# Kernel tuning notes

Measured on AMD Instinct MI355X. Metric: run time of the kernel, lower is better.

The kernel has to match this reference:

```python
import jax, jax.numpy as jnp
import numpy as np

N_NODES = 100000
N_EDGES = 1600000
IN_DIM = 128
HID_DIM = 64
OUT_DIM = 64


def setup_inputs() -> dict:
    key = jax.random.key(0)
    ks = jax.random.split(key, 8)
    x = jax.random.normal(ks[0], (N_NODES, IN_DIM), dtype=jnp.float32)
    edge_index = jax.random.randint(ks[1], (2, N_EDGES), 0, N_NODES, dtype=jnp.int64)
    edge_weight = jax.random.uniform(ks[2], (N_EDGES,), dtype=jnp.float32)  # cached PPMI values
    # Glorot-style params for the two PPMIConv layers
    W1 = jax.random.normal(ks[3], (IN_DIM, HID_DIM), dtype=jnp.float32) * (1.0 / np.sqrt(IN_DIM))
    b1 = jnp.zeros((HID_DIM,), dtype=jnp.float32)
    W2 = jax.random.normal(ks[4], (HID_DIM, OUT_DIM), dtype=jnp.float32) * (1.0 / np.sqrt(HID_DIM))
    b2 = jnp.zeros((OUT_DIM,), dtype=jnp.float32)
    return {"x": x, "edge_index": edge_index, "edge_weight": edge_weight,
            "W1": W1, "b1": b1, "W2": W2, "b2": b2}


def _gcn_norm(edge_index, edge_weight, num_nodes):
    # symmetric normalization of (PPMI) edge weights: D^{-1/2} A D^{-1/2}
    row, col = edge_index[0], edge_index[1]
    deg = jax.ops.segment_sum(edge_weight, row, num_segments=num_nodes)
    deg_inv_sqrt = jnp.where(deg > 0, jax.lax.rsqrt(jnp.maximum(deg, 1e-12)), 0.0)
    return deg_inv_sqrt[row] * edge_weight * deg_inv_sqrt[col]


def _ppmi_conv(x, W, b, edge_index, norm, num_nodes):
    h = x @ W                                   # [N, D_out] transform
    msg = h[edge_index[0]] * norm[:, None]      # [E, D_out] gather + weight
    out = jax.ops.segment_sum(msg, edge_index[1], num_segments=num_nodes)  # scatter-add
    return out + b


def reference(x, edge_index, edge_weight, W1, b1, W2, b2):
    n = x.shape[0]
    norm = _gcn_norm(edge_index, edge_weight, n)
    h = _ppmi_conv(x, W1, b1, edge_index, norm, n)
    h = jax.nn.relu(h)
    h = _ppmi_conv(h, W2, b2, edge_index, norm, n)
    return h
```

## Files before the change

kernel.cpp:

```cpp
#include <hip/hip_runtime.h>
#include <hip/hip_fp16.h>

#define N_NODES 100000
#define N_EDGES 1600000
#define IN_DIM 128
#define HID_DIM 64
#define OUT_DIM 64
#define NBKT 196
#define BSH 9
#define BMSK 511
#define NBLK 512
#define CHUNK 3125
#define MROW (NBKT * NBLK)

typedef _Float16 half8 __attribute__((ext_vector_type(8)));
typedef float f32x4 __attribute__((ext_vector_type(4)));

__global__ void count_kernel(const int* __restrict__ rows, const int* __restrict__ cols,
                             int* __restrict__ M) {
    __shared__ unsigned hc[NBKT], hr[NBKT];
    for (int i = threadIdx.x; i < NBKT; i += 256) { hc[i] = 0; hr[i] = 0; }
    __syncthreads();
    const int s = blockIdx.x * CHUNK;
    const int e = min(s + CHUNK, N_EDGES);
    for (int i = s + threadIdx.x; i < e; i += 256) {
        atomicAdd(&hr[rows[i] >> BSH], 1u);
        atomicAdd(&hc[cols[i] >> BSH], 1u);
    }
    __syncthreads();
    for (int i = threadIdx.x; i < NBKT; i += 256) {
        M[i * NBLK + blockIdx.x] = (int)hc[i];
        M[MROW + i * NBLK + blockIdx.x] = (int)hr[i];
    }
}

__global__ void block_sum_kernel(const int* __restrict__ counts, int* __restrict__ partials, int n) {
    __shared__ int sh[256];
    int base = blockIdx.x * 1024;
    int s = 0;
    for (int i = threadIdx.x; i < 1024; i += 256) {
        int idx = base + i;
        s += (idx < n) ? counts[idx] : 0;
    }
    sh[threadIdx.x] = s;
    __syncthreads();
    for (int off = 128; off > 0; off >>= 1) {
        if (threadIdx.x < off) sh[threadIdx.x] += sh[threadIdx.x + off];
        __syncthreads();
    }
    if (threadIdx.x == 0) partials[blockIdx.x] = sh[0];
}

__global__ void scan_partials_kernel(int* __restrict__ p, int nb) {
    __shared__ int sh[256];
    int t = threadIdx.x;
    int v = (t < nb) ? p[t] : 0;
    sh[t] = v;
    __syncthreads();
    for (int off = 1; off < 256; off <<= 1) {
        int add = (t >= off) ? sh[t - off] : 0;
        __syncthreads();
        sh[t] += add;
        __syncthreads();
    }
    if (t < nb) p[t] = sh[t] - v;
}

__global__ void scan_final_kernel(const int* __restrict__ counts, const int* __restrict__ partials,
                                  int* __restrict__ offsets, int n) {
    __shared__ int sh[256];
    int t = threadIdx.x;
    int idx0 = blockIdx.x * 1024 + t * 4;
    int v[4];
    int s = 0;
#pragma unroll
    for (int j = 0; j < 4; ++j) {
        int id = idx0 + j;
        v[j] = (id < n) ? counts[id] : 0;
        s += v[j];
    }
    sh[t] = s;
    __syncthreads();
    for (int off = 1; off < 256; off <<= 1) {
        int add = (t >= off) ? sh[t - off] : 0;
        __syncthreads();
        sh[t] += add;
        __syncthreads();
    }
    int run = sh[t] - s + partials[blockIdx.x];
#pragma unroll
    for (int j = 0; j < 4; ++j) {
        int id = idx0 + j;
        if (id < n) offsets[id] = run;
        run += v[j];
    }
    if (idx0 <= n - 1 && n - 1 < idx0 + 4) offsets[n] = run;
}

__global__ __launch_bounds__(256) void scatter_kernel(
        const int* __restrict__ rows, const int* __restrict__ cols,
        const float* __restrict__ w, const int* __restrict__ M, const int* __restrict__ Ms,
        unsigned long long* __restrict__ pkA, unsigned* __restrict__ pkR) {
    __shared__ unsigned long long pay[CHUNK];
    __shared__ unsigned char bkt[CHUNK + 3];
    __shared__ unsigned scn[256];
    __shared__ unsigned base[NBKT], cur[NBKT], gbase[NBKT];
    const int blk = blockIdx.x, t = threadIdx.x;
    const int s = blk * CHUNK;

    unsigned cnt = (t < NBKT) ? (unsigned)M[t * NBLK + blk] : 0;
    scn[t] = cnt;
    __syncthreads();
    for (int off = 1; off < 256; off <<= 1) {
        unsigned a = (t >= off) ? scn[t - off] : 0;
        __syncthreads();
        scn[t] += a;
        __syncthreads();
    }
    if (t < NBKT) {
        unsigned b0 = scn[t] - cnt;
        base[t] = b0; cur[t] = b0;
        gbase[t] = (unsigned)Ms[t * NBLK + blk];
    }
    __syncthreads();
    for (int i = s + t; i < s + CHUNK; i += 256) {
        int r = rows[i], c = cols[i];
        unsigned b = (unsigned)c >> BSH;
        unsigned p = atomicAdd(&cur[b], 1u);
        pay[p] = ((unsigned long long)__float_as_uint(w[i]) << 32) |
                 (unsigned)(((c & BMSK) << 17) | r);
        bkt[p] = (unsigned char)b;
    }
    __syncthreads();
    for (int i = t; i < CHUNK; i += 256) {
        unsigned b = bkt[i];
        pkA[gbase[b] + (i - base[b])] = pay[i];
    }
    __syncthreads();

    cnt = (t < NBKT) ? (unsigned)M[MROW + t * NBLK + blk] : 0;
    scn[t] = cnt;
    __syncthreads();
    for (int off = 1; off < 256; off <<= 1) {
        unsigned a = (t >= off) ? scn[t - off] : 0;
        __syncthreads();
        scn[t] += a;
        __syncthreads();
    }
    if (t < NBKT) {
        unsigned b0 = scn[t] - cnt;
        base[t] = b0; cur[t] = b0;
        gbase[t] = (unsigned)Ms[MROW + t * NBLK + blk] - (unsigned)N_EDGES;
    }
    __syncthreads();
    unsigned* pay32 = (unsigned*)pay;
    for (int i = s + t; i < s + CHUNK; i += 256) {
        int r = rows[i];
        unsigned b = (unsigned)r >> BSH;
        unsigned p = atomicAdd(&cur[b], 1u);
        unsigned short hw = __half_as_ushort(__float2half(w[i]));
        pay32[p] = ((unsigned)hw << 16) | (unsigned)(r & BMSK);
        bkt[p] = (unsigned char)b;
    }
    __syncthreads();
    for (int i = t; i < CHUNK; i += 256) {
        unsigned b = bkt[i];
        pkR[gbase[b] + (i - base[b])] = pay32[i];
    }
}

__global__ void deg_reduce_kernel(const unsigned* __restrict__ pkR,
                                  const int* __restrict__ Ms, float* __restrict__ dis) {
    __shared__ float acc[512];
    const int b = blockIdx.x;
    const int t = threadIdx.x;
    acc[t] = 0.f; acc[t + 256] = 0.f;
    __syncthreads();
    const int s = Ms[MROW + b * NBLK] - N_EDGES;
    const int e = Ms[MROW + (b + 1) * NBLK] - N_EDGES;
    for (int i = s + t; i < e; i += 256) {
        unsigned u = pkR[i];
        float wv = __half2float(__ushort_as_half((unsigned short)(u >> 16)));
        atomicAdd(&acc[u & (unsigned)BMSK], wv);
    }
    __syncthreads();
#pragma unroll
    for (int k = 0; k < 2; ++k) {
        int node = b * 512 + t + k * 256;
        if (node < N_NODES) {
            float d = acc[t + k * 256];
            dis[node] = d > 0.f ? rsqrtf(fmaxf(d, 1e-12f)) : 0.f;
        }
    }
}

__global__ void fill_kernel(const unsigned long long* __restrict__ pk,
                            const int* __restrict__ Ms,
                            int2* __restrict__ csr, int* __restrict__ offsets) {
    __shared__ unsigned hist[512];
    __shared__ unsigned pairs[256];
    const int b = blockIdx.x;
    const int t = threadIdx.x;
    hist[t] = 0; hist[t + 256] = 0;
    __syncthreads();
    const int s = Ms[b * NBLK];
    const int e = Ms[(b + 1) * NBLK];
    for (int i = s + t; i < e; i += 256) {
        unsigned lo = (unsigned)pk[i];
        atomicAdd(&hist[(lo >> 17) & (unsigned)BMSK], 1u);
    }
    __syncthreads();
    unsigned h0 = hist[2 * t], h1 = hist[2 * t + 1];
    pairs[t] = h0 + h1;
    __syncthreads();
    for (int off = 1; off < 256; off <<= 1) {
        unsigned add = (t >= off) ? pairs[t - off] : 0;
        __syncthreads();
        pairs[t] += add;
        __syncthreads();
    }
    unsigned P = pairs[t] - (h0 + h1) + (unsigned)s;
    unsigned e0 = P, e1 = P + h0;
    int n0 = b * 512 + 2 * t;
    int n1 = n0 + 1;
    if (n0 <= N_NODES) offsets[n0] = (int)e0;
    if (n1 <= N_NODES) offsets[n1] = (int)e1;
    hist[2 * t] = e0; hist[2 * t + 1] = e1;
    __syncthreads();
    for (int i = s + t; i < e; i += 256) {
        unsigned long long p = pk[i];
        unsigned lo = (unsigned)p;
        unsigned cl = (lo >> 17) & (unsigned)BMSK;
        int r = (int)(lo & 0x1FFFFu);
        unsigned pos = atomicAdd(&hist[cl], 1u);
        csr[pos] = make_int2(r, (int)(unsigned)(p >> 32));
    }
}

__global__ void wfrag_kernel(const float* __restrict__ W1, const float* __restrict__ W2,
                             __half* __restrict__ F1, __half* __restrict__ F2) {
    int t = blockIdx.x * 256 + threadIdx.x;
    if (t < 1024) {
        int lane = t & 63, fg = t >> 6;
        int col = (fg & 3) * 16 + (lane & 15);
        int kb = (fg >> 2) * 32 + (lane >> 4) * 8;
        __half v[8];
#pragma unroll
        for (int j = 0; j < 8; ++j) v[j] = __float2half(W1[(kb + j) * 64 + col]);
        *reinterpret_cast<uint4*>(F1 + (size_t)t * 8) = *reinterpret_cast<uint4*>(v);
    } else if (t < 1536) {
        int u = t - 1024;
        int lane = u & 63, fg = u >> 6;
        int col = (fg & 3) * 16 + (lane & 15);
        int kb = (fg >> 2) * 32 + (lane >> 4) * 8;
        __half v[8];
#pragma unroll
        for (int j = 0; j < 8; ++j) v[j] = __float2half(W2[(kb + j) * 64 + col]);
        *reinterpret_cast<uint4*>(F2 + (size_t)u * 8) = *reinterpret_cast<uint4*>(v);
    }
}

__global__ __launch_bounds__(256) void gemm1_mfma(
        const float* __restrict__ x, const __half* __restrict__ F1,
        const float* __restrict__ dis, __half* __restrict__ h1) {
    const int wid = threadIdx.x >> 6, lane = threadIdx.x & 63;
    const int row0 = blockIdx.x * 64 + wid * 16;
    int arow = min(row0 + (lane & 15), N_NODES - 1);
    const int kb0 = (lane >> 4) * 8;
    const float* ap = x + (size_t)arow * 128 + kb0;

    f32x4 acc[4] = {};
#pragma unroll
    for (int c = 0; c < 4; ++c) {
        float4 a0 = *reinterpret_cast<const float4*>(ap + c * 32);
        float4 a1 = *reinterpret_cast<const float4*>(ap + c * 32 + 4);
        half8 af;
        af[0] = (_Float16)a0.x; af[1] = (_Float16)a0.y; af[2] = (_Float16)a0.z; af[3] = (_Float16)a0.w;
        af[4] = (_Float16)a1.x; af[5] = (_Float16)a1.y; af[6] = (_Float16)a1.z; af[7] = (_Float16)a1.w;
#pragma unroll
        for (int ct = 0; ct < 4; ++ct) {
            half8 bf = *reinterpret_cast<const half8*>(F1 + ((size_t)(c * 4 + ct) * 64 + lane) * 8);
            acc[ct] = __builtin_amdgcn_mfma_f32_16x16x32_f16(af, bf, acc[ct], 0, 0, 0);
        }
    }
    const int prow = row0 + ((lane >> 4) << 2);
    const int col = lane & 15;
#pragma unroll
    for (int r = 0; r < 4; ++r) {
        int rr = prow + r;
        if (rr < N_NODES) {
            float dv = dis[rr];
#pragma unroll
            for (int ct = 0; ct < 4; ++ct)
                h1[(size_t)rr * 64 + ct * 16 + col] = __float2half(acc[ct][r] * dv);
        }
    }
}

__global__ __launch_bounds__(256) void gemm2_mfma(
        const __half* __restrict__ g, const __half* __restrict__ F2,
        const float* __restrict__ b2, float* __restrict__ out) {
    const int wid = threadIdx.x >> 6, lane = threadIdx.x & 63;
    const int row0 = blockIdx.x * 64 + wid * 16;
    int arow = min(row0 + (lane & 15), N_NODES - 1);
    const int kb0 = (lane >> 4) * 8;
    const __half* ap = g + (size_t)arow * 64 + kb0;

    f32x4 acc[4] = {};
#pragma unroll
    for (int c = 0; c < 2; ++c) {
        half8 af = *reinterpret_cast<const half8*>(ap + c * 32);
#pragma unroll
        for (int ct = 0; ct < 4; ++ct) {
            half8 bf = *reinterpret_cast<const half8*>(F2 + ((size_t)(c * 4 + ct) * 64 + lane) * 8);
            acc[ct] = __builtin_amdgcn_mfma_f32_16x16x32_f16(af, bf, acc[ct], 0, 0, 0);
        }
    }
    const int prow = row0 + ((lane >> 4) << 2);
    const int col = lane & 15;
#pragma unroll
    for (int ct = 0; ct < 4; ++ct) {
        float bb = b2[ct * 16 + col];
#pragma unroll
        for (int r = 0; r < 4; ++r) {
            int rr = prow + r;
            if (rr < N_NODES) out[(size_t)rr * 64 + ct * 16 + col] = acc[ct][r] + bb;
        }
    }
}

template <int BIAS_RELU>
__global__ __launch_bounds__(512) void gather_vec_kernel(
        const __half* __restrict__ h, const int2* __restrict__ csr,
        const int* __restrict__ offsets, const float* __restrict__ bias,
        const float* __restrict__ dis, __half* __restrict__ outh, int n) {
    int node = blockIdx.x * 8 + (threadIdx.x >> 6);
    int lane = threadIdx.x & 63;
    int q = lane & 7;
    int g = lane >> 3;
    int s = offsets[node];
    int e = offsets[node + 1];

    float a0 = 0.f, a1 = 0.f, a2 = 0.f, a3 = 0.f, a4 = 0.f, a5 = 0.f, a6 = 0.f, a7 = 0.f;
    for (int j = s; j < e; j += 16) {
        int eA = j + g;
        int eB = j + 8 + g;
        int2 pA = csr[min(eA, e - 1)];
        int2 pB = csr[min(eB, e - 1)];
        float nA = (eA < e) ? __int_as_float(pA.y) : 0.f;
        float nB = (eB < e) ? __int_as_float(pB.y) : 0.f;
        uint4 uA = *reinterpret_cast<const uint4*>(h + ((size_t)pA.x << 6) + (q << 3));
        uint4 uB = *reinterpret_cast<const uint4*>(h + ((size_t)pB.x << 6) + (q << 3));
        float2 f;
        f = __half22float2(__builtin_bit_cast(__half2, uA.x)); a0 = fmaf(f.x, nA, a0); a1 = fmaf(f.y, nA, a1);
        f = __half22float2(__builtin_bit_cast(__half2, uA.y)); a2 = fmaf(f.x, nA, a2); a3 = fmaf(f.y, nA, a3);
        f = __half22float2(__builtin_bit_cast(__half2, uA.z)); a4 = fmaf(f.x, nA, a4); a5 = fmaf(f.y, nA, a5);
        f = __half22float2(__builtin_bit_cast(__half2, uA.w)); a6 = fmaf(f.x, nA, a6); a7 = fmaf(f.y, nA, a7);
        f = __half22float2(__builtin_bit_cast(__half2, uB.x)); a0 = fmaf(f.x, nB, a0); a1 = fmaf(f.y, nB, a1);
        f = __half22float2(__builtin_bit_cast(__half2, uB.y)); a2 = fmaf(f.x, nB, a2); a3 = fmaf(f.y, nB, a3);
        f = __half22float2(__builtin_bit_cast(__half2, uB.z)); a4 = fmaf(f.x, nB, a4); a5 = fmaf(f.y, nB, a5);
        f = __half22float2(__builtin_bit_cast(__half2, uB.w)); a6 = fmaf(f.x, nB, a6); a7 = fmaf(f.y, nB, a7);
    }
#pragma unroll
    for (int m = 8; m <= 32; m <<= 1) {
        a0 += __shfl_xor(a0, m); a1 += __shfl_xor(a1, m);
        a2 += __shfl_xor(a2, m); a3 += __shfl_xor(a3, m);
        a4 += __shfl_xor(a4, m); a5 += __shfl_xor(a5, m);
        a6 += __shfl_xor(a6, m); a7 += __shfl_xor(a7, m);
    }
    if (g == 0) {
        float dv = dis[node];
        if (BIAS_RELU) {
            const float4 b0 = *reinterpret_cast<const float4*>(bias + (q << 3));
            const float4 b1 = *reinterpret_cast<const float4*>(bias + (q << 3) + 4);
            a0 = fmaxf(fmaf(a0, dv, b0.x), 0.f) * dv; a1 = fmaxf(fmaf(a1, dv, b0.y), 0.f) * dv;
            a2 = fmaxf(fmaf(a2, dv, b0.z), 0.f) * dv; a3 = fmaxf(fmaf(a3, dv, b0.w), 0.f) * dv;
            a4 = fmaxf(fmaf(a4, dv, b1.x), 0.f) * dv; a5 = fmaxf(fmaf(a5, dv, b1.y), 0.f) * dv;
            a6 = fmaxf(fmaf(a6, dv, b1.z), 0.f) * dv; a7 = fmaxf(fmaf(a7, dv, b1.w), 0.f) * dv;
        } else {
            a0 *= dv; a1 *= dv; a2 *= dv; a3 *= dv;
            a4 *= dv; a5 *= dv; a6 *= dv; a7 *= dv;
        }
        __half2 o0 = __float22half2_rn(make_float2(a0, a1));
        __half2 o1 = __float22half2_rn(make_float2(a2, a3));
        __half2 o2 = __float22half2_rn(make_float2(a4, a5));
        __half2 o3 = __float22half2_rn(make_float2(a6, a7));
        uint4 u = make_uint4(__builtin_bit_cast(unsigned, o0), __builtin_bit_cast(unsigned, o1),
                             __builtin_bit_cast(unsigned, o2), __builtin_bit_cast(unsigned, o3));
        *reinterpret_cast<uint4*>(outh + ((size_t)node << 6) + (q << 3)) = u;
    }
}

extern "C" void kernel_launch(void* const* d_in, const int* in_sizes, int n_in,
                              void* d_out, int out_size, void* d_ws, size_t ws_size,
                              hipStream_t stream) {
    const float* x  = (const float*)d_in[0];
    const int*   ei = (const int*)d_in[1];
    const float* ew = (const float*)d_in[2];
    const float* W1 = (const float*)d_in[3];
    const float* b1 = (const float*)d_in[4];
    const float* W2 = (const float*)d_in[5];
    const float* b2 = (const float*)d_in[6];
    float* out = (float*)d_out;
    char*  ws  = (char*)d_ws;

    const int* rows = ei;
    const int* cols = ei + N_EDGES;

    int2*     csr      = (int2*)(ws + 0);
    unsigned long long* pkA = (unsigned long long*)(ws + 12800000);
    unsigned* pkR      = (unsigned*)(ws + 25600000);
    __half*   h1       = (__half*)(ws + 12800000);
    __half*   g        = (__half*)(ws + 12800000);
    __half*   t        = (__half*)(ws + 25600000);
    int*      M        = (int*)(ws + 38400000);
    int*      Ms       = (int*)(ws + 39202816);
    int*      partials = (int*)(ws + 40005636);
    int*      offsets  = (int*)(ws + 40006424);
    float*    dis      = (float*)(ws + 40406428);
    __half*   F1       = (__half*)(ws + 40806432);
    __half*   F2       = (__half*)(ws + 40822816);

    const int TPB = 256;
    const int n2  = 2 * MROW;
    const int nSB2 = (n2 + 1023) / 1024;

    wfrag_kernel<<<6, TPB, 0, stream>>>(W1, W2, F1, F2);

    count_kernel<<<NBLK, TPB, 0, stream>>>(rows, cols, M);

    block_sum_kernel<<<nSB2, 256, 0, stream>>>(M, partials, n2);
    scan_partials_kernel<<<1, 256, 0, stream>>>(partials, nSB2);
    scan_final_kernel<<<nSB2, 256, 0, stream>>>(M, partials, Ms, n2);

    scatter_kernel<<<NBLK, TPB, 0, stream>>>(rows, cols, ew, M, Ms, pkA, pkR);

    deg_reduce_kernel<<<NBKT, TPB, 0, stream>>>(pkR, Ms, dis);

    fill_kernel<<<NBKT, TPB, 0, stream>>>(pkA, Ms, csr, offsets);

    gemm1_mfma<<<(N_NODES + 63) / 64, TPB, 0, stream>>>(x, F1, dis, h1);

    gather_vec_kernel<1><<<N_NODES / 8, 512, 0, stream>>>(h1, csr, offsets, b1, dis, t, N_NODES);

    gather_vec_kernel<0><<<N_NODES / 8, 512, 0, stream>>>(t, csr, offsets, b1, dis, g, N_NODES);

    gemm2_mfma<<<(N_NODES + 63) / 64, TPB, 0, stream>>>(g, F2, b2, out);
}
```

Measured before the change: 193.8 us.

## Fuse weight-fragment prep into count, merge fill and degree kernels, vectorize loads

Folds the W1/W2 fp16 fragment preparation into extra blocks of the count kernel and merges the degree-reduce and CSR-fill kernels into one launch, removing two kernel launches. It switches edge chunking to 500 blocks of 3200 edges so rows, cols and weights can be read as int4/float4. The gather loop gets an unpredicated main body for full 16-edge groups plus a masked tail. Workspace offsets are recomputed for the smaller bucket matrix.

```diff
diff --git a/kernel.cpp b/kernel.cpp
--- a/kernel.cpp
+++ b/kernel.cpp
@@ -9,23 +9,50 @@
 #define NBKT 196
 #define BSH 9
 #define BMSK 511
-#define NBLK 512
-#define CHUNK 3125
+#define NBLK 500
+#define CHUNK 3200
 #define MROW (NBKT * NBLK)
 
 typedef _Float16 half8 __attribute__((ext_vector_type(8)));
 typedef float f32x4 __attribute__((ext_vector_type(4)));
 
 __global__ void count_kernel(const int* __restrict__ rows, const int* __restrict__ cols,
-                             int* __restrict__ M) {
+                             int* __restrict__ M,
+                             const float* __restrict__ W1, const float* __restrict__ W2,
+                             __half* __restrict__ F1, __half* __restrict__ F2) {
     __shared__ unsigned hc[NBKT], hr[NBKT];
+    if (blockIdx.x >= NBLK) {
+        int t = (blockIdx.x - NBLK) * 256 + threadIdx.x;
+        if (t < 1024) {
+            int lane = t & 63, fg = t >> 6;
+            int col = (fg & 3) * 16 + (lane & 15);
+            int kb = (fg >> 2) * 32 + (lane >> 4) * 8;
+            __half v[8];
+#pragma unroll
+            for (int j = 0; j < 8; ++j) v[j] = __float2half(W1[(kb + j) * 64 + col]);
+            *reinterpret_cast<uint4*>(F1 + (size_t)t * 8) = *reinterpret_cast<uint4*>(v);
+        } else if (t < 1536) {
+            int u = t - 1024;
+            int lane = u & 63, fg = u >> 6;
+            int col = (fg & 3) * 16 + (lane & 15);
+            int kb = (fg >> 2) * 32 + (lane >> 4) * 8;
+            __half v[8];
+#pragma unroll
+            for (int j = 0; j < 8; ++j) v[j] = __float2half(W2[(kb + j) * 64 + col]);
+            *reinterpret_cast<uint4*>(F2 + (size_t)u * 8) = *reinterpret_cast<uint4*>(v);
+        }
+        return;
+    }
     for (int i = threadIdx.x; i < NBKT; i += 256) { hc[i] = 0; hr[i] = 0; }
     __syncthreads();
-    const int s = blockIdx.x * CHUNK;
-    const int e = min(s + CHUNK, N_EDGES);
-    for (int i = s + threadIdx.x; i < e; i += 256) {
-        atomicAdd(&hr[rows[i] >> BSH], 1u);
-        atomicAdd(&hc[cols[i] >> BSH], 1u);
+    const int4* r4 = (const int4*)(rows + blockIdx.x * CHUNK);
+    const int4* c4 = (const int4*)(cols + blockIdx.x * CHUNK);
+    for (int i = threadIdx.x; i < CHUNK / 4; i += 256) {
+        int4 r = r4[i], c = c4[i];
+        atomicAdd(&hr[r.x >> BSH], 1u); atomicAdd(&hr[r.y >> BSH], 1u);
+        atomicAdd(&hr[r.z >> BSH], 1u); atomicAdd(&hr[r.w >> BSH], 1u);
+        atomicAdd(&hc[c.x >> BSH], 1u); atomicAdd(&hc[c.y >> BSH], 1u);
+        atomicAdd(&hc[c.z >> BSH], 1u); atomicAdd(&hc[c.w >> BSH], 1u);
     }
     __syncthreads();
     for (int i = threadIdx.x; i < NBKT; i += 256) {
@@ -102,11 +129,14 @@
         const float* __restrict__ w, const int* __restrict__ M, const int* __restrict__ Ms,
         unsigned long long* __restrict__ pkA, unsigned* __restrict__ pkR) {
     __shared__ unsigned long long pay[CHUNK];
-    __shared__ unsigned char bkt[CHUNK + 3];
+    __shared__ unsigned char bkt[CHUNK];
     __shared__ unsigned scn[256];
     __shared__ unsigned base[NBKT], cur[NBKT], gbase[NBKT];
     const int blk = blockIdx.x, t = threadIdx.x;
     const int s = blk * CHUNK;
+    const int4* r4 = (const int4*)(rows + s);
+    const int4* c4 = (const int4*)(cols + s);
+    const float4* w4 = (const float4*)(w + s);
 
     unsigned cnt = (t < NBKT) ? (unsigned)M[t * NBLK + blk] : 0;
     scn[t] = cnt;
@@ -123,13 +153,15 @@
         gbase[t] = (unsigned)Ms[t * NBLK + blk];
     }
     __syncthreads();
-    for (int i = s + t; i < s + CHUNK; i += 256) {
-        int r = rows[i], c = cols[i];
-        unsigned b = (unsigned)c >> BSH;
-        unsigned p = atomicAdd(&cur[b], 1u);
-        pay[p] = ((unsigned long long)__float_as_uint(w[i]) << 32) |
-                 (unsigned)(((c & BMSK) << 17) | r);
-        bkt[p] = (unsigned char)b;
+#define PUTA(RV, CV, WV) { unsigned b = (unsigned)(CV) >> BSH; \
+        unsigned p = atomicAdd(&cur[b], 1u); \
+        pay[p] = ((unsigned long long)__float_as_uint(WV) << 32) | \
+                 (unsigned)((((CV) & BMSK) << 17) | (RV)); \
+        bkt[p] = (unsigned char)b; }
+    for (int i = t; i < CHUNK / 4; i += 256) {
+        int4 rr = r4[i]; int4 cc = c4[i]; float4 ww = w4[i];
+        PUTA(rr.x, cc.x, ww.x); PUTA(rr.y, cc.y, ww.y);
+        PUTA(rr.z, cc.z, ww.z); PUTA(rr.w, cc.w, ww.w);
     }
     __syncthreads();
     for (int i = t; i < CHUNK; i += 256) {
@@ -154,13 +186,13 @@
     }
     __syncthreads();
     unsigned* pay32 = (unsigned*)pay;
-    for (int i = s + t; i < s + CHUNK; i += 256) {
-        int r = rows[i];
-        unsigned b = (unsigned)r >> BSH;
-        unsigned p = atomicAdd(&cur[b], 1u);
-        unsigned short hw = __half_as_ushort(__float2half(w[i]));
-        pay32[p] = ((unsigned)hw << 16) | (unsigned)(r & BMSK);
-        bkt[p] = (unsigned char)b;
+#define PUTR(RV, WV) { unsigned b = (unsigned)(RV) >> BSH; \
+        unsigned p = atomicAdd(&cur[b], 1u); \
+        pay32[p] = ((unsigned)__half_as_ushort(__float2half(WV)) << 16) | (unsigned)((RV) & BMSK); \
+        bkt[p] = (unsigned char)b; }
+    for (int i = t; i < CHUNK / 4; i += 256) {
+        int4 rr = r4[i]; float4 ww = w4[i];
+        PUTR(rr.x, ww.x); PUTR(rr.y, ww.y); PUTR(rr.z, ww.z); PUTR(rr.w, ww.w);
     }
     __syncthreads();
     for (int i = t; i < CHUNK; i += 256) {
@@ -169,94 +201,71 @@
     }
 }
 
-__global__ void deg_reduce_kernel(const unsigned* __restrict__ pkR,
-                                  const int* __restrict__ Ms, float* __restrict__ dis) {
-    __shared__ float acc[512];
-    const int b = blockIdx.x;
+__global__ __launch_bounds__(256) void fill_deg_kernel(
+        const unsigned long long* __restrict__ pkA, const unsigned* __restrict__ pkR,
+        const int* __restrict__ Ms, int2* __restrict__ csr,
+        int* __restrict__ offsets, float* __restrict__ dis) {
+    __shared__ unsigned sh[768];
     const int t = threadIdx.x;
-    acc[t] = 0.f; acc[t + 256] = 0.f;
-    __syncthreads();
-    const int s = Ms[MROW + b * NBLK] - N_EDGES;
-    const int e = Ms[MROW + (b + 1) * NBLK] - N_EDGES;
-    for (int i = s + t; i < e; i += 256) {
-        unsigned u = pkR[i];
-        float wv = __half2float(__ushort_as_half((unsigned short)(u >> 16)));
-        atomicAdd(&acc[u & (unsigned)BMSK], wv);
-    }
-    __syncthreads();
-#pragma unroll
-    for (int k = 0; k < 2; ++k) {
-        int node = b * 512 + t + k * 256;
-        if (node < N_NODES) {
-            float d = acc[t + k * 256];
-            dis[node] = d > 0.f ? rsqrtf(fmaxf(d, 1e-12f)) : 0.f;
-        }
-    }
-}
-
-__global__ void fill_kernel(const unsigned long long* __restrict__ pk,
-                            const int* __restrict__ Ms,
-                            int2* __restrict__ csr, int* __restrict__ offsets) {
-    __shared__ unsigned hist[512];
-    __shared__ unsigned pairs[256];
-    const int b = blockIdx.x;
-    const int t = threadIdx.x;
-    hist[t] = 0; hist[t + 256] = 0;
-    __syncthreads();
-    const int s = Ms[b * NBLK];
-    const int e = Ms[(b + 1) * NBLK];
-    for (int i = s + t; i < e; i += 256) {
-        unsigned lo = (unsigned)pk[i];
-        atomicAdd(&hist[(lo >> 17) & (unsigned)BMSK], 1u);
-    }
-    __syncthreads();
-    unsigned h0 = hist[2 * t], h1 = hist[2 * t + 1];
-    pairs[t] = h0 + h1;
-    __syncthreads();
-    for (int off = 1; off < 256; off <<= 1) {
-        unsigned add = (t >= off) ? pairs[t - off] : 0;
-        __syncthreads();
-        pairs[t] += add;
-        __syncthreads();
-    }
-    unsigned P = pairs[t] - (h0 + h1) + (unsigned)s;
-    unsigned e0 = P, e1 = P + h0;
-    int n0 = b * 512 + 2 * t;
-    int n1 = n0 + 1;
-    if (n0 <= N_NODES) offsets[n0] = (int)e0;
-    if (n1 <= N_NODES) offsets[n1] = (int)e1;
-    hist[2 * t] = e0; hist[2 * t + 1] = e1;
-    __syncthreads();
-    for (int i = s + t; i < e; i += 256) {
-        unsigned long long p = pk[i];
-        unsigned lo = (unsigned)p;
-        unsigned cl = (lo >> 17) & (unsigned)BMSK;
-        int r = (int)(lo & 0x1FFFFu);
-        unsigned pos = atomicAdd(&hist[cl], 1u);
-        csr[pos] = make_int2(r, (int)(unsigned)(p >> 32));
-    }
-}
-
-__global__ void wfrag_kernel(const float* __restrict__ W1, const float* __restrict__ W2,
-                             __half* __restrict__ F1, __half* __restrict__ F2) {
-    int t = blockIdx.x * 256 + threadIdx.x;
-    if (t < 1024) {
-        int lane = t & 63, fg = t >> 6;
-        int col = (fg & 3) * 16 + (lane & 15);
-        int kb = (fg >> 2) * 32 + (lane >> 4) * 8;
-        __half v[8];
-#pragma unroll
-        for (int j = 0; j < 8; ++j) v[j] = __float2half(W1[(kb + j) * 64 + col]);
-        *reinterpret_cast<uint4*>(F1 + (size_t)t * 8) = *reinterpret_cast<uint4*>(v);
-    } else if (t < 1536) {
-        int u = t - 1024;
-        int lane = u & 63, fg = u >> 6;
-        int col = (fg & 3) * 16 + (lane & 15);
-        int kb = (fg >> 2) * 32 + (lane >> 4) * 8;
-        __half v[8];
-#pragma unroll
-        for (int j = 0; j < 8; ++j) v[j] = __float2half(W2[(kb + j) * 64 + col]);
-        *reinterpret_cast<uint4*>(F2 + (size_t)u * 8) = *reinterpret_cast<uint4*>(v);
+    if (blockIdx.x < NBKT) {
+        unsigned* hist = sh;
+        unsigned* pairs = sh + 512;
+        const int b = blockIdx.x;
+        hist[t] = 0; hist[t + 256] = 0;
+        __syncthreads();
+        const int s = Ms[b * NBLK];
+        const int e = Ms[(b + 1) * NBLK];
+        for (int i = s + t; i < e; i += 256) {
+            unsigned lo = (unsigned)pkA[i];
+            atomicAdd(&hist[(lo >> 17) & (unsigned)BMSK], 1u);
+        }
+        __syncthreads();
+        unsigned h0 = hist[2 * t], h1 = hist[2 * t + 1];
+        pairs[t] = h0 + h1;
+        __syncthreads();
+        for (int off = 1; off < 256; off <<= 1) {
+            unsigned add = (t >= off) ? pairs[t - off] : 0;
+            __syncthreads();
+            pairs[t] += add;
+            __syncthreads();
+        }
+        unsigned P = pairs[t] - (h0 + h1) + (unsigned)s;
+        unsigned e0 = P, e1 = P + h0;
+        int n0 = b * 512 + 2 * t;
+        int n1 = n0 + 1;
+        if (n0 <= N_NODES) offsets[n0] = (int)e0;
+        if (n1 <= N_NODES) offsets[n1] = (int)e1;
+        hist[2 * t] = e0; hist[2 * t + 1] = e1;
+        __syncthreads();
+        for (int i = s + t; i < e; i += 256) {
+            unsigned long long p = pkA[i];
+            unsigned lo = (unsigned)p;
+            unsigned cl = (lo >> 17) & (unsigned)BMSK;
+            int r = (int)(lo & 0x1FFFFu);
+            unsigned pos = atomicAdd(&hist[cl], 1u);
+            csr[pos] = make_int2(r, (int)(unsigned)(p >> 32));
+        }
+    } else {
+        float* acc = (float*)sh;
+        const int b = blockIdx.x - NBKT;
+        acc[t] = 0.f; acc[t + 256] = 0.f;
+        __syncthreads();
+        const int s = Ms[MROW + b * NBLK] - N_EDGES;
+        const int e = Ms[MROW + (b + 1) * NBLK] - N_EDGES;
+        for (int i = s + t; i < e; i += 256) {
+            unsigned u = pkR[i];
+            float wv = __half2float(__ushort_as_half((unsigned short)(u >> 16)));
+            atomicAdd(&acc[u & (unsigned)BMSK], wv);
+        }
+        __syncthreads();
+#pragma unroll
+        for (int k = 0; k < 2; ++k) {
+            int node = b * 512 + t + k * 256;
+            if (node < N_NODES) {
+                float d = acc[t + k * 256];
+                dis[node] = d > 0.f ? rsqrtf(fmaxf(d, 1e-12f)) : 0.f;
+            }
+        }
     }
 }
 
@@ -342,25 +351,40 @@
     int e = offsets[node + 1];
 
     float a0 = 0.f, a1 = 0.f, a2 = 0.f, a3 = 0.f, a4 = 0.f, a5 = 0.f, a6 = 0.f, a7 = 0.f;
-    for (int j = s; j < e; j += 16) {
-        int eA = j + g;
-        int eB = j + 8 + g;
-        int2 pA = csr[min(eA, e - 1)];
-        int2 pB = csr[min(eB, e - 1)];
-        float nA = (eA < e) ? __int_as_float(pA.y) : 0.f;
-        float nB = (eB < e) ? __int_as_float(pB.y) : 0.f;
+#define FMA8(U, NV) { float2 f_; \
+    f_ = __half22float2(__builtin_bit_cast(__half2, (U).x)); a0 = fmaf(f_.x, NV, a0); a1 = fmaf(f_.y, NV, a1); \
+    f_ = __half22float2(__builtin_bit_cast(__half2, (U).y)); a2 = fmaf(f_.x, NV, a2); a3 = fmaf(f_.y, NV, a3); \
+    f_ = __half22float2(__builtin_bit_cast(__half2, (U).z)); a4 = fmaf(f_.x, NV, a4); a5 = fmaf(f_.y, NV, a5); \
+    f_ = __half22float2(__builtin_bit_cast(__half2, (U).w)); a6 = fmaf(f_.x, NV, a6); a7 = fmaf(f_.y, NV, a7); }
+
+    int j = s;
+    for (; j + 16 <= e; j += 16) {
+        int2 pA = csr[j + g];
+        int2 pB = csr[j + 8 + g];
         uint4 uA = *reinterpret_cast<const uint4*>(h + ((size_t)pA.x << 6) + (q << 3));
         uint4 uB = *reinterpret_cast<const uint4*>(h + ((size_t)pB.x << 6) + (q << 3));
-        float2 f;
-        f = __half22float2(__builtin_bit_cast(__half2, uA.x)); a0 = fmaf(f.x, nA, a0); a1 = fmaf(f.y, nA, a1);
-        f = __half22float2(__builtin_bit_cast(__half2, uA.y)); a2 = fmaf(f.x, nA, a2); a3 = fmaf(f.y, nA, a3);
-        f = __half22float2(__builtin_bit_cast(__half2, uA.z)); a4 = fmaf(f.x, nA, a4); a5 = fmaf(f.y, nA, a5);
-        f = __half22float2(__builtin_bit_cast(__half2, uA.w)); a6 = fmaf(f.x, nA, a6); a7 = fmaf(f.y, nA, a7);
-        f = __half22float2(__builtin_bit_cast(__half2, uB.x)); a0 = fmaf(f.x, nB, a0); a1 = fmaf(f.y, nB, a1);
-        f = __half22float2(__builtin_bit_cast(__half2, uB.y)); a2 = fmaf(f.x, nB, a2); a3 = fmaf(f.y, nB, a3);
-        f = __half22float2(__builtin_bit_cast(__half2, uB.z)); a4 = fmaf(f.x, nB, a4); a5 = fmaf(f.y, nB, a5);
-        f = __half22float2(__builtin_bit_cast(__half2, uB.w)); a6 = fmaf(f.x, nB, a6); a7 = fmaf(f.y, nB, a7);
-    }
+        float nA = __int_as_float(pA.y);
+        float nB = __int_as_float(pB.y);
+        FMA8(uA, nA); FMA8(uB, nB);
+    }
+    int rem = e - j;
+    if (rem > 8) {
+        int eB = j + 8 + g;
+        int2 pA = csr[j + g];
+        int2 pB = csr[min(eB, e - 1)];
+        uint4 uA = *reinterpret_cast<const uint4*>(h + ((size_t)pA.x << 6) + (q << 3));
+        uint4 uB = *reinterpret_cast<const uint4*>(h + ((size_t)pB.x << 6) + (q << 3));
+        float nA = __int_as_float(pA.y);
+        float nB = (eB < e) ? __int_as_float(pB.y) : 0.f;
+        FMA8(uA, nA); FMA8(uB, nB);
+    } else if (rem > 0) {
+        int eA = j + g;
+        int2 pA = csr[min(eA, e - 1)];
+        uint4 uA = *reinterpret_cast<const uint4*>(h + ((size_t)pA.x << 6) + (q << 3));
+        float nA = (eA < e) ? __int_as_float(pA.y) : 0.f;
+        FMA8(uA, nA);
+    }
+#undef FMA8
 #pragma unroll
     for (int m = 8; m <= 32; m <<= 1) {
         a0 += __shfl_xor(a0, m); a1 += __shfl_xor(a1, m);
@@ -414,20 +438,18 @@
     __half*   g        = (__half*)(ws + 12800000);
     __half*   t        = (__half*)(ws + 25600000);
     int*      M        = (int*)(ws + 38400000);
-    int*      Ms       = (int*)(ws + 39202816);
-    int*      partials = (int*)(ws + 40005636);
-    int*      offsets  = (int*)(ws + 40006424);
-    float*    dis      = (float*)(ws + 40406428);
-    __half*   F1       = (__half*)(ws + 40806432);
-    __half*   F2       = (__half*)(ws + 40822816);
+    int*      Ms       = (int*)(ws + 39184000);
+    int*      partials = (int*)(ws + 39968016);
+    int*      offsets  = (int*)(ws + 39968784);
+    float*    dis      = (float*)(ws + 40368800);
+    __half*   F1       = (__half*)(ws + 40768800);
+    __half*   F2       = (__half*)(ws + 40785184);
 
     const int TPB = 256;
     const int n2  = 2 * MROW;
     const int nSB2 = (n2 + 1023) / 1024;
 
-    wfrag_kernel<<<6, TPB, 0, stream>>>(W1, W2, F1, F2);
-
-    count_kernel<<<NBLK, TPB, 0, stream>>>(rows, cols, M);
+    count_kernel<<<NBLK + 6, TPB, 0, stream>>>(rows, cols, M, W1, W2, F1, F2);
 
     block_sum_kernel<<<nSB2, 256, 0, stream>>>(M, partials, n2);
     scan_partials_kernel<<<1, 256, 0, stream>>>(partials, nSB2);
@@ -435,9 +457,7 @@
 
     scatter_kernel<<<NBLK, TPB, 0, stream>>>(rows, cols, ew, M, Ms, pkA, pkR);
 
-    deg_reduce_kernel<<<NBKT, TPB, 0, stream>>>(pkR, Ms, dis);
-
-    fill_kernel<<<NBKT, TPB, 0, stream>>>(pkA, Ms, csr, offsets);
+    fill_deg_kernel<<<2 * NBKT, TPB, 0, stream>>>(pkA, pkR, Ms, csr, offsets, dis);
 
     gemm1_mfma<<<(N_NODES + 63) / 64, TPB, 0, stream>>>(x, F1, dis, h1);
 
```

Measured after the change: 165.8 us. 14.4% less time.
